# Kernel tuning notes

Measured on AMD Instinct MI355X. Metric: run time of the kernel, lower is better.

## Reference

```python
import jax, jax.numpy as jnp
import numpy as np

N = 100000   # nodes
E = 1600000  # edges per relation (avg in-degree 16)
D = 128      # gcn_hidden (in_feat == out_feat)
R = 2        # relations: forward_edge, backward_edge


def setup_inputs() -> dict:
    key = jax.random.key(0)
    ks = jax.random.split(key, 8)
    x = jax.random.normal(ks[0], (N, D), dtype=jnp.float32)
    src_fwd = jax.random.randint(ks[1], (E,), 0, N, dtype=jnp.int32)
    dst_fwd = jax.random.randint(ks[2], (E,), 0, N, dtype=jnp.int32)
    src_bwd = jax.random.randint(ks[3], (E,), 0, N, dtype=jnp.int32)
    dst_bwd = jax.random.randint(ks[4], (E,), 0, N, dtype=jnp.int32)
    # xavier_uniform with relu gain sqrt(2)
    gain = np.sqrt(2.0)
    lim_rel = gain * np.sqrt(6.0 / (D + D))
    rel_weight = jax.random.uniform(ks[5], (R, D, D), minval=-lim_rel, maxval=lim_rel, dtype=jnp.float32)
    loop_weight = jax.random.uniform(ks[6], (D, D), minval=-lim_rel, maxval=lim_rel, dtype=jnp.float32)
    h_bias = jnp.zeros((D,), dtype=jnp.float32)
    return {
        'x': x,
        'src_fwd': src_fwd, 'dst_fwd': dst_fwd,
        'src_bwd': src_bwd, 'dst_bwd': dst_bwd,
        'rel_weight': rel_weight, 'loop_weight': loop_weight, 'h_bias': h_bias,
    }


def _rel_conv(x, src, dst, W):
    # dgl GraphConv(norm='right', weight per relation): scatter-sum src feats to
    # dst, divide by clamped in-degree, then matmul W (in_feat == out_feat so
    # order of matmul vs aggregation is mathematically equivalent).
    msg = x[src]                                            # [E, D] gather
    agg = jax.ops.segment_sum(msg, dst, num_segments=N)     # [N, D] scatter-add
    deg = jax.ops.segment_sum(jnp.ones((src.shape[0],), x.dtype), dst, num_segments=N)
    agg = agg / jnp.clip(deg, 1.0)[:, None]                 # right norm, deg clamp(min=1)
    return agg @ W                                          # [N, D]


def reference(x, src_fwd, dst_fwd, src_bwd, dst_bwd, rel_weight, loop_weight, h_bias):
    h = _rel_conv(x, src_fwd, dst_fwd, rel_weight[0])
    h = h + _rel_conv(x, src_bwd, dst_bwd, rel_weight[1])   # HeteroGraphConv sums per-relation results
    h = h + x @ loop_weight                                 # self loop
    h = h + h_bias                                          # bias
    h = jax.nn.relu(h)                                      # activation
    return h                                                # dropout is identity in eval
```

## Files before the change

### kernel.cpp

```cpp
#include <hip/hip_runtime.h>
#include <hip/hip_bf16.h>


#define DFEAT 128
#define CH2 4096
#define PSH 6
#define NBMAX 3200
#define CAPB 1536
#define NPACK 24

typedef __attribute__((ext_vector_type(8))) short short8v;
typedef __attribute__((ext_vector_type(4))) float float4v;
typedef __attribute__((ext_vector_type(2))) unsigned int u2v;
typedef __attribute__((ext_vector_type(4))) unsigned short ushort4v;

__global__ __launch_bounds__(256) void front_kernel(
        const float4v* __restrict__ x4, ushort4v* __restrict__ xb4, int n4,
        const int* __restrict__ src0, const int* __restrict__ dst0,
        const int* __restrict__ src1, const int* __restrict__ dst1,
        int* __restrict__ cursor, unsigned* __restrict__ binned,
        const float* __restrict__ wrel, const float* __restrict__ wloop,
        unsigned short* __restrict__ wb,
        int N, int E, int nbin) {
    __shared__ unsigned cntp[NBMAX / 2];
    __shared__ int base[NBMAX];
    int tid = threadIdx.x;
    int bid = blockIdx.x;

    if (bid < nbin) {
        auto ldp = [&](int i) {
            int r = (i >= E) ? 1 : 0;
            int e = i - r * E;
            int t = r ? dst1[e] : dst0[e];
            return r * N + t;
        };
        auto lds_ = [&](int i) {
            int r = (i >= E) ? 1 : 0;
            int e = i - r * E;
            return r ? src1[e] : src0[e];
        };
        for (int i = tid; i < NBMAX / 2; i += 256) cntp[i] = 0;
        __syncthreads();
        int lo = bid * CH2, hi = min(2 * E, lo + CH2);
        for (int ii = lo + tid; ii < hi; ii += 1024) {
            int p0 = ldp(ii);
            int p1 = (ii + 256 < hi) ? ldp(ii + 256) : -1;
            int p2 = (ii + 512 < hi) ? ldp(ii + 512) : -1;
            int p3 = (ii + 768 < hi) ? ldp(ii + 768) : -1;
            int b0 = p0 >> PSH;
            atomicAdd(&cntp[b0 >> 1], (b0 & 1) ? 0x10000u : 1u);
            if (p1 >= 0) { int b1 = p1 >> PSH; atomicAdd(&cntp[b1 >> 1], (b1 & 1) ? 0x10000u : 1u); }
            if (p2 >= 0) { int b2 = p2 >> PSH; atomicAdd(&cntp[b2 >> 1], (b2 & 1) ? 0x10000u : 1u); }
            if (p3 >= 0) { int b3 = p3 >> PSH; atomicAdd(&cntp[b3 >> 1], (b3 & 1) ? 0x10000u : 1u); }
        }
        __syncthreads();
        for (int b = tid; b < NBMAX; b += 256) {
            int c = (int)((cntp[b >> 1] >> ((b & 1) * 16)) & 0xFFFFu);
            if (c) base[b] = b * CAPB + atomicAdd(&cursor[b], c);
        }
        __syncthreads();
        for (int ii = lo + tid; ii < hi; ii += 1024) {
            int p0 = ldp(ii);             int s0 = lds_(ii);
            int i1 = ii + 256, i2 = ii + 512, i3 = ii + 768;
            int p1 = (i1 < hi) ? ldp(i1) : -1;  int s1 = (i1 < hi) ? lds_(i1) : 0;
            int p2 = (i2 < hi) ? ldp(i2) : -1;  int s2 = (i2 < hi) ? lds_(i2) : 0;
            int p3 = (i3 < hi) ? ldp(i3) : -1;  int s3 = (i3 < hi) ? lds_(i3) : 0;
            { int slot = atomicAdd(&base[p0 >> PSH], 1);
              binned[slot] = ((unsigned)(p0 & 63) << 17) | (unsigned)s0; }
            if (p1 >= 0) { int slot = atomicAdd(&base[p1 >> PSH], 1);
                           binned[slot] = ((unsigned)(p1 & 63) << 17) | (unsigned)s1; }
            if (p2 >= 0) { int slot = atomicAdd(&base[p2 >> PSH], 1);
                           binned[slot] = ((unsigned)(p2 & 63) << 17) | (unsigned)s2; }
            if (p3 >= 0) { int slot = atomicAdd(&base[p3 >> PSH], 1);
                           binned[slot] = ((unsigned)(p3 & 63) << 17) | (unsigned)s3; }
        }
    } else if (bid < nbin + NPACK) {
        int t = (bid - nbin) * 256 + tid;
        if (t < 12 * 8 * 64) {
            int lane = t & 63;
            int kbase = (t >> 9) * 32 + (lane >> 4) * 8;
            int col = (((t >> 6) & 7) << 4) + (lane & 15);
            unsigned short tmp[8];
#pragma unroll
            for (int j = 0; j < 8; ++j) {
                int k = kbase + j;
                float v = (k < 256) ? wrel[k * DFEAT + col]
                                    : wloop[(k - 256) * DFEAT + col];
                tmp[j] = __hip_bfloat16_raw(__float2bfloat16(v)).x;
            }
            *(ushort4*)(wb + t * 8)     = make_ushort4(tmp[0], tmp[1], tmp[2], tmp[3]);
            *(ushort4*)(wb + t * 8 + 4) = make_ushort4(tmp[4], tmp[5], tmp[6], tmp[7]);
        }
    } else {
        int cb = bid - nbin - NPACK;
#pragma unroll
        for (int k = 0; k < 4; ++k) {
            int i = cb * 1024 + k * 256 + tid;
            if (i < n4) {
                float4v v = __builtin_nontemporal_load(x4 + i);
                ushort4v o;
                o[0] = __hip_bfloat16_raw(__float2bfloat16(v[0])).x;
                o[1] = __hip_bfloat16_raw(__float2bfloat16(v[1])).x;
                o[2] = __hip_bfloat16_raw(__float2bfloat16(v[2])).x;
                o[3] = __hip_bfloat16_raw(__float2bfloat16(v[3])).x;
                xb4[i] = o;
            }
        }
    }
}

#define CONSUME(Q0, Q1, Q2, Q3) {                                              \
    a[0] += __uint_as_float(Q0[0] << 16) + __uint_as_float(Q1[0] << 16)        \
          + __uint_as_float(Q2[0] << 16) + __uint_as_float(Q3[0] << 16);       \
    a[1] += __uint_as_float(Q0[0] & 0xffff0000u) + __uint_as_float(Q1[0] & 0xffff0000u) \
          + __uint_as_float(Q2[0] & 0xffff0000u) + __uint_as_float(Q3[0] & 0xffff0000u); \
    a[2] += __uint_as_float(Q0[1] << 16) + __uint_as_float(Q1[1] << 16)        \
          + __uint_as_float(Q2[1] << 16) + __uint_as_float(Q3[1] << 16);       \
    a[3] += __uint_as_float(Q0[1] & 0xffff0000u) + __uint_as_float(Q1[1] & 0xffff0000u) \
          + __uint_as_float(Q2[1] & 0xffff0000u) + __uint_as_float(Q3[1] & 0xffff0000u); }

__global__ __launch_bounds__(128) void agg_kernel(
        const u2v* __restrict__ xb2,
        const unsigned* __restrict__ binned,
        const int* __restrict__ cursor,
        unsigned short* __restrict__ aggb, int N, int M) {
    __shared__ unsigned ebuf[CAPB];
    __shared__ int cnt[64], cur[64], rs[64];
    int tid = threadIdx.x;
    int b = blockIdx.x;
    int total = min(cursor[b], CAPB);
    const unsigned* seg = binned + (size_t)b * CAPB;
    int P0 = b << PSH;
    int hw = tid >> 5, lane = tid & 31;

    if (tid < 64) cnt[tid] = 0;
    __syncthreads();
    for (int i = tid; i < total; i += 128)
        atomicAdd(&cnt[seg[i] >> 17], 1);
    __syncthreads();
    if (tid < 64) {
        int c = cnt[tid];
        int inc = c;
#pragma unroll
        for (int off = 1; off < 64; off <<= 1) {
            int t2 = __shfl_up(inc, off);
            if (tid >= off) inc += t2;
        }
        rs[tid] = inc - c;
        cur[tid] = inc - c;
    }
    __syncthreads();
    for (int i = tid; i < total; i += 128) {
        unsigned v = seg[i];
        int slot = atomicAdd(&cur[v >> 17], 1);
        ebuf[slot] = v & 0x1FFFFu;
    }
    __syncthreads();

    for (int pi = 0; pi < 16; ++pi) {
        int pl = hw * 16 + pi;
        int s0 = rs[pl], c = cnt[pl];
        float4v a = (float4v){0.f, 0.f, 0.f, 0.f};
        int e = 0;
        if (c >= 8) {
            u2v A0 = xb2[(size_t)ebuf[s0]     * 32 + lane];
            u2v B0 = xb2[(size_t)ebuf[s0 + 1] * 32 + lane];
            u2v C0 = xb2[(size_t)ebuf[s0 + 2] * 32 + lane];
            u2v D0 = xb2[(size_t)ebuf[s0 + 3] * 32 + lane];
            u2v A1 = xb2[(size_t)ebuf[s0 + 4] * 32 + lane];
            u2v B1 = xb2[(size_t)ebuf[s0 + 5] * 32 + lane];
            u2v C1 = xb2[(size_t)ebuf[s0 + 6] * 32 + lane];
            u2v D1 = xb2[(size_t)ebuf[s0 + 7] * 32 + lane];
            for (e = 8; e + 4 <= c; e += 4) {
                u2v nA = xb2[(size_t)ebuf[s0 + e]     * 32 + lane];
                u2v nB = xb2[(size_t)ebuf[s0 + e + 1] * 32 + lane];
                u2v nC = xb2[(size_t)ebuf[s0 + e + 2] * 32 + lane];
                u2v nD = xb2[(size_t)ebuf[s0 + e + 3] * 32 + lane];
                CONSUME(A0, B0, C0, D0);
                A0 = A1; B0 = B1; C0 = C1; D0 = D1;
                A1 = nA; B1 = nB; C1 = nC; D1 = nD;
            }
            CONSUME(A0, B0, C0, D0);
            CONSUME(A1, B1, C1, D1);
        } else if (c >= 4) {
            u2v A0 = xb2[(size_t)ebuf[s0]     * 32 + lane];
            u2v B0 = xb2[(size_t)ebuf[s0 + 1] * 32 + lane];
            u2v C0 = xb2[(size_t)ebuf[s0 + 2] * 32 + lane];
            u2v D0 = xb2[(size_t)ebuf[s0 + 3] * 32 + lane];
            CONSUME(A0, B0, C0, D0);
            e = 4;
        }
        for (; e < c; ++e) {
            int s = ebuf[s0 + e];
            u2v g = xb2[(size_t)s * 32 + lane];
            a[0] += __uint_as_float(g[0] << 16);
            a[1] += __uint_as_float(g[0] & 0xffff0000u);
            a[2] += __uint_as_float(g[1] << 16);
            a[3] += __uint_as_float(g[1] & 0xffff0000u);
        }
        int pg = P0 + pl;
        if (pg < M) {
            float inv = 1.0f / (float)max(c, 1);
            ushort4v w;
            w[0] = __hip_bfloat16_raw(__float2bfloat16(a[0] * inv)).x;
            w[1] = __hip_bfloat16_raw(__float2bfloat16(a[1] * inv)).x;
            w[2] = __hip_bfloat16_raw(__float2bfloat16(a[2] * inv)).x;
            w[3] = __hip_bfloat16_raw(__float2bfloat16(a[3] * inv)).x;
            __builtin_nontemporal_store(
                w, (ushort4v*)(aggb + (size_t)pg * DFEAT + 4 * lane));
        }
    }
}

__global__ __launch_bounds__(256) void mfma_gemm_kernel(
        const unsigned short* __restrict__ aggb,
        const unsigned short* __restrict__ xb,
        const unsigned short* __restrict__ wb,
        const float* __restrict__ bias,
        float* __restrict__ out, int N) {
    int tid = threadIdx.x;
    int wv = tid >> 6, lane = tid & 63;
    int R0 = blockIdx.x * 128 + wv * 32;
    int mrow = lane & 15, quad = lane >> 4;

    float4v acc[2][8];
#pragma unroll
    for (int rt = 0; rt < 2; ++rt)
#pragma unroll
        for (int ct = 0; ct < 8; ++ct) acc[rt][ct] = (float4v){0.f, 0.f, 0.f, 0.f};

    int n0 = min(R0 + mrow, N - 1);
    int n1 = min(R0 + 16 + mrow, N - 1);

#pragma unroll
    for (int kc = 0; kc < 12; ++kc) {
        int off = (kc & 3) * 32 + quad * 8;
        const unsigned short* s0;
        const unsigned short* s1;
        if (kc < 4)      { s0 = aggb + (size_t)n0 * DFEAT;       s1 = aggb + (size_t)n1 * DFEAT; }
        else if (kc < 8) { s0 = aggb + (size_t)(N + n0) * DFEAT; s1 = aggb + (size_t)(N + n1) * DFEAT; }
        else             { s0 = xb + (size_t)n0 * DFEAT;         s1 = xb + (size_t)n1 * DFEAT; }
        short8v a0 = *(const short8v*)(s0 + off);
        short8v a1 = *(const short8v*)(s1 + off);
#pragma unroll
        for (int ct = 0; ct < 8; ++ct) {
            short8v bfr = *(const short8v*)(wb + (((kc * 8 + ct) << 6) + lane) * 8);
            acc[0][ct] = __builtin_amdgcn_mfma_f32_16x16x32_bf16(a0, bfr, acc[0][ct], 0, 0, 0);
            acc[1][ct] = __builtin_amdgcn_mfma_f32_16x16x32_bf16(a1, bfr, acc[1][ct], 0, 0, 0);
        }
    }

#pragma unroll
    for (int ct = 0; ct < 8; ++ct) {
        int col = ct * 16 + mrow;
        float bv = bias[col];
#pragma unroll
        for (int rt = 0; rt < 2; ++rt) {
#pragma unroll
            for (int i = 0; i < 4; ++i) {
                int row = R0 + rt * 16 + quad * 4 + i;
                if (row < N)
                    __builtin_nontemporal_store(fmaxf(acc[rt][ct][i] + bv, 0.f),
                                                out + (size_t)row * DFEAT + col);
            }
        }
    }
}

extern "C" void kernel_launch(void* const* d_in, const int* in_sizes, int n_in,
                              void* d_out, int out_size, void* d_ws, size_t ws_size,
                              hipStream_t stream) {
    const float* x      = (const float*)d_in[0];
    const int* src_fwd  = (const int*)d_in[1];
    const int* dst_fwd  = (const int*)d_in[2];
    const int* src_bwd  = (const int*)d_in[3];
    const int* dst_bwd  = (const int*)d_in[4];
    const float* wrel   = (const float*)d_in[5];
    const float* wloop  = (const float*)d_in[6];
    const float* hbias  = (const float*)d_in[7];
    float* out          = (float*)d_out;

    int N = in_sizes[0] / DFEAT;
    int E = in_sizes[1];
    int M = 2 * N;
    int TE = 2 * E;
    int NB = (M + 63) / 64;

    unsigned short* wb   = (unsigned short*)d_ws;
    unsigned* binned     = (unsigned*)(wb + 12 * 8 * 64 * 8);
    unsigned short* xb   = (unsigned short*)(binned + (size_t)NB * CAPB);
    unsigned short* aggb = xb + (size_t)(N + 1) * DFEAT;
    int* cursor          = (int*)(aggb + (size_t)M * DFEAT);

    int n4 = N * (DFEAT / 4);
    int nconv = (n4 + 1023) / 1024;
    int nbin = (TE + CH2 - 1) / CH2;

    (void)hipMemsetAsync(cursor, 0, NB * sizeof(int), stream);

    front_kernel<<<nbin + NPACK + nconv, 256, 0, stream>>>(
        (const float4v*)x, (ushort4v*)xb, n4,
        src_fwd, dst_fwd, src_bwd, dst_bwd,
        cursor, binned, wrel, wloop, wb, N, E, nbin);

    agg_kernel<<<NB, 128, 0, stream>>>(
        (const u2v*)xb, binned, cursor, aggb, N, M);

    mfma_gemm_kernel<<<(N + 127) / 128, 256, 0, stream>>>(
        aggb, xb, wb, hbias, out, N);
}
```

Before: 345.6 us.

## Fuse neighbor aggregation with MFMA GEMM via shared-memory tile

Merges the aggregation and GEMM kernels into one kernel. Each block handles 64 nodes: for each relation it aggregates the bin into an LDS bf16 tile, then runs MFMA against that relation's weights, and finally adds the self-loop term from xb. The bf16 aggregate buffer is no longer written to or read back from global memory, and one launch is removed. In exchange each block has more serial phases and barriers, grid size falls to about 1563 blocks of 256 threads, and the per-row relation padding changes to Npad so bins align with node tiles.

```diff
diff --git a/kernel.cpp b/kernel.cpp
--- a/kernel.cpp
+++ b/kernel.cpp
@@ -21,7 +21,7 @@
         int* __restrict__ cursor, unsigned* __restrict__ binned,
         const float* __restrict__ wrel, const float* __restrict__ wloop,
         unsigned short* __restrict__ wb,
-        int N, int E, int nbin) {
+        int Np, int E, int nbin) {
     __shared__ unsigned cntp[NBMAX / 2];
     __shared__ int base[NBMAX];
     int tid = threadIdx.x;
@@ -32,7 +32,7 @@
             int r = (i >= E) ? 1 : 0;
             int e = i - r * E;
             int t = r ? dst1[e] : dst0[e];
-            return r * N + t;
+            return r * Np + t;
         };
         auto lds_ = [&](int i) {
             int r = (i >= E) ? 1 : 0;
@@ -119,134 +119,128 @@
     a[3] += __uint_as_float(Q0[1] & 0xffff0000u) + __uint_as_float(Q1[1] & 0xffff0000u) \
           + __uint_as_float(Q2[1] & 0xffff0000u) + __uint_as_float(Q3[1] & 0xffff0000u); }
 
-__global__ __launch_bounds__(128) void agg_kernel(
+__global__ __launch_bounds__(256) void aggmm_kernel(
         const u2v* __restrict__ xb2,
+        const unsigned short* __restrict__ xb,
         const unsigned* __restrict__ binned,
         const int* __restrict__ cursor,
-        unsigned short* __restrict__ aggb, int N, int M) {
+        const unsigned short* __restrict__ wb,
+        const float* __restrict__ bias,
+        float* __restrict__ out, int N, int NBH) {
     __shared__ unsigned ebuf[CAPB];
+    __shared__ __align__(16) unsigned short Atile[64][136];
     __shared__ int cnt[64], cur[64], rs[64];
     int tid = threadIdx.x;
-    int b = blockIdx.x;
-    int total = min(cursor[b], CAPB);
-    const unsigned* seg = binned + (size_t)b * CAPB;
-    int P0 = b << PSH;
+    int g = blockIdx.x;
     int hw = tid >> 5, lane = tid & 31;
-
-    if (tid < 64) cnt[tid] = 0;
-    __syncthreads();
-    for (int i = tid; i < total; i += 128)
-        atomicAdd(&cnt[seg[i] >> 17], 1);
-    __syncthreads();
-    if (tid < 64) {
-        int c = cnt[tid];
-        int inc = c;
-#pragma unroll
-        for (int off = 1; off < 64; off <<= 1) {
-            int t2 = __shfl_up(inc, off);
-            if (tid >= off) inc += t2;
-        }
-        rs[tid] = inc - c;
-        cur[tid] = inc - c;
-    }
-    __syncthreads();
-    for (int i = tid; i < total; i += 128) {
-        unsigned v = seg[i];
-        int slot = atomicAdd(&cur[v >> 17], 1);
-        ebuf[slot] = v & 0x1FFFFu;
-    }
-    __syncthreads();
-
-    for (int pi = 0; pi < 16; ++pi) {
-        int pl = hw * 16 + pi;
-        int s0 = rs[pl], c = cnt[pl];
-        float4v a = (float4v){0.f, 0.f, 0.f, 0.f};
-        int e = 0;
-        if (c >= 8) {
-            u2v A0 = xb2[(size_t)ebuf[s0]     * 32 + lane];
-            u2v B0 = xb2[(size_t)ebuf[s0 + 1] * 32 + lane];
-            u2v C0 = xb2[(size_t)ebuf[s0 + 2] * 32 + lane];
-            u2v D0 = xb2[(size_t)ebuf[s0 + 3] * 32 + lane];
-            u2v A1 = xb2[(size_t)ebuf[s0 + 4] * 32 + lane];
-            u2v B1 = xb2[(size_t)ebuf[s0 + 5] * 32 + lane];
-            u2v C1 = xb2[(size_t)ebuf[s0 + 6] * 32 + lane];
-            u2v D1 = xb2[(size_t)ebuf[s0 + 7] * 32 + lane];
-            for (e = 8; e + 4 <= c; e += 4) {
-                u2v nA = xb2[(size_t)ebuf[s0 + e]     * 32 + lane];
-                u2v nB = xb2[(size_t)ebuf[s0 + e + 1] * 32 + lane];
-                u2v nC = xb2[(size_t)ebuf[s0 + e + 2] * 32 + lane];
-                u2v nD = xb2[(size_t)ebuf[s0 + e + 3] * 32 + lane];
+    int wv = tid >> 6, l64 = tid & 63;
+    int mrow = l64 & 15, quad = l64 >> 4;
+
+    float4v acc[8];
+#pragma unroll
+    for (int ct = 0; ct < 8; ++ct) acc[ct] = (float4v){0.f, 0.f, 0.f, 0.f};
+
+    for (int rel = 0; rel < 2; ++rel) {
+        int b = rel ? (NBH + g) : g;
+        int total = min(cursor[b], CAPB);
+        const unsigned* seg = binned + (size_t)b * CAPB;
+
+        if (tid < 64) cnt[tid] = 0;
+        __syncthreads();
+        for (int i = tid; i < total; i += 256)
+            atomicAdd(&cnt[seg[i] >> 17], 1);
+        __syncthreads();
+        if (tid < 64) {
+            int c = cnt[tid];
+            int inc = c;
+#pragma unroll
+            for (int off = 1; off < 64; off <<= 1) {
+                int t2 = __shfl_up(inc, off);
+                if (tid >= off) inc += t2;
+            }
+            rs[tid] = inc - c;
+            cur[tid] = inc - c;
+        }
+        __syncthreads();
+        for (int i = tid; i < total; i += 256) {
+            unsigned v = seg[i];
+            int slot = atomicAdd(&cur[v >> 17], 1);
+            ebuf[slot] = v & 0x1FFFFu;
+        }
+        __syncthreads();
+
+        for (int pi = 0; pi < 8; ++pi) {
+            int pl = hw * 8 + pi;
+            int s0 = rs[pl], c = cnt[pl];
+            float4v a = (float4v){0.f, 0.f, 0.f, 0.f};
+            int e = 0;
+            if (c >= 8) {
+                u2v A0 = xb2[(size_t)ebuf[s0]     * 32 + lane];
+                u2v B0 = xb2[(size_t)ebuf[s0 + 1] * 32 + lane];
+                u2v C0 = xb2[(size_t)ebuf[s0 + 2] * 32 + lane];
+                u2v D0 = xb2[(size_t)ebuf[s0 + 3] * 32 + lane];
+                u2v A1 = xb2[(size_t)ebuf[s0 + 4] * 32 + lane];
+                u2v B1 = xb2[(size_t)ebuf[s0 + 5] * 32 + lane];
+                u2v C1 = xb2[(size_t)ebuf[s0 + 6] * 32 + lane];
+                u2v D1 = xb2[(size_t)ebuf[s0 + 7] * 32 + lane];
+                for (e = 8; e + 4 <= c; e += 4) {
+                    u2v nA = xb2[(size_t)ebuf[s0 + e]     * 32 + lane];
+                    u2v nB = xb2[(size_t)ebuf[s0 + e + 1] * 32 + lane];
+                    u2v nC = xb2[(size_t)ebuf[s0 + e + 2] * 32 + lane];
+                    u2v nD = xb2[(size_t)ebuf[s0 + e + 3] * 32 + lane];
+                    CONSUME(A0, B0, C0, D0);
+                    A0 = A1; B0 = B1; C0 = C1; D0 = D1;
+                    A1 = nA; B1 = nB; C1 = nC; D1 = nD;
+                }
                 CONSUME(A0, B0, C0, D0);
-                A0 = A1; B0 = B1; C0 = C1; D0 = D1;
-                A1 = nA; B1 = nB; C1 = nC; D1 = nD;
-            }
-            CONSUME(A0, B0, C0, D0);
-            CONSUME(A1, B1, C1, D1);
-        } else if (c >= 4) {
-            u2v A0 = xb2[(size_t)ebuf[s0]     * 32 + lane];
-            u2v B0 = xb2[(size_t)ebuf[s0 + 1] * 32 + lane];
-            u2v C0 = xb2[(size_t)ebuf[s0 + 2] * 32 + lane];
-            u2v D0 = xb2[(size_t)ebuf[s0 + 3] * 32 + lane];
-            CONSUME(A0, B0, C0, D0);
-            e = 4;
-        }
-        for (; e < c; ++e) {
-            int s = ebuf[s0 + e];
-            u2v g = xb2[(size_t)s * 32 + lane];
-            a[0] += __uint_as_float(g[0] << 16);
-            a[1] += __uint_as_float(g[0] & 0xffff0000u);
-            a[2] += __uint_as_float(g[1] << 16);
-            a[3] += __uint_as_float(g[1] & 0xffff0000u);
-        }
-        int pg = P0 + pl;
-        if (pg < M) {
+                CONSUME(A1, B1, C1, D1);
+            } else if (c >= 4) {
+                u2v A0 = xb2[(size_t)ebuf[s0]     * 32 + lane];
+                u2v B0 = xb2[(size_t)ebuf[s0 + 1] * 32 + lane];
+                u2v C0 = xb2[(size_t)ebuf[s0 + 2] * 32 + lane];
+                u2v D0 = xb2[(size_t)ebuf[s0 + 3] * 32 + lane];
+                CONSUME(A0, B0, C0, D0);
+                e = 4;
+            }
+            for (; e < c; ++e) {
+                int s = ebuf[s0 + e];
+                u2v gq = xb2[(size_t)s * 32 + lane];
+                a[0] += __uint_as_float(gq[0] << 16);
+                a[1] += __uint_as_float(gq[0] & 0xffff0000u);
+                a[2] += __uint_as_float(gq[1] << 16);
+                a[3] += __uint_as_float(gq[1] & 0xffff0000u);
+            }
             float inv = 1.0f / (float)max(c, 1);
             ushort4v w;
             w[0] = __hip_bfloat16_raw(__float2bfloat16(a[0] * inv)).x;
             w[1] = __hip_bfloat16_raw(__float2bfloat16(a[1] * inv)).x;
             w[2] = __hip_bfloat16_raw(__float2bfloat16(a[2] * inv)).x;
             w[3] = __hip_bfloat16_raw(__float2bfloat16(a[3] * inv)).x;
-            __builtin_nontemporal_store(
-                w, (ushort4v*)(aggb + (size_t)pg * DFEAT + 4 * lane));
-        }
-    }
-}
-
-__global__ __launch_bounds__(256) void mfma_gemm_kernel(
-        const unsigned short* __restrict__ aggb,
-        const unsigned short* __restrict__ xb,
-        const unsigned short* __restrict__ wb,
-        const float* __restrict__ bias,
-        float* __restrict__ out, int N) {
-    int tid = threadIdx.x;
-    int wv = tid >> 6, lane = tid & 63;
-    int R0 = blockIdx.x * 128 + wv * 32;
-    int mrow = lane & 15, quad = lane >> 4;
-
-    float4v acc[2][8];
-#pragma unroll
-    for (int rt = 0; rt < 2; ++rt)
-#pragma unroll
-        for (int ct = 0; ct < 8; ++ct) acc[rt][ct] = (float4v){0.f, 0.f, 0.f, 0.f};
-
-    int n0 = min(R0 + mrow, N - 1);
-    int n1 = min(R0 + 16 + mrow, N - 1);
-
-#pragma unroll
-    for (int kc = 0; kc < 12; ++kc) {
-        int off = (kc & 3) * 32 + quad * 8;
-        const unsigned short* s0;
-        const unsigned short* s1;
-        if (kc < 4)      { s0 = aggb + (size_t)n0 * DFEAT;       s1 = aggb + (size_t)n1 * DFEAT; }
-        else if (kc < 8) { s0 = aggb + (size_t)(N + n0) * DFEAT; s1 = aggb + (size_t)(N + n1) * DFEAT; }
-        else             { s0 = xb + (size_t)n0 * DFEAT;         s1 = xb + (size_t)n1 * DFEAT; }
-        short8v a0 = *(const short8v*)(s0 + off);
-        short8v a1 = *(const short8v*)(s1 + off);
+            *(ushort4v*)&Atile[pl][4 * lane] = w;
+        }
+        __syncthreads();
+
+#pragma unroll
+        for (int kc4 = 0; kc4 < 4; ++kc4) {
+            int kc = rel * 4 + kc4;
+            short8v a0 = *(const short8v*)&Atile[wv * 16 + mrow][kc4 * 32 + quad * 8];
+#pragma unroll
+            for (int ct = 0; ct < 8; ++ct) {
+                short8v bfr = *(const short8v*)(wb + (((kc * 8 + ct) << 6) + l64) * 8);
+                acc[ct] = __builtin_amdgcn_mfma_f32_16x16x32_bf16(a0, bfr, acc[ct], 0, 0, 0);
+            }
+        }
+        __syncthreads();
+    }
+
+    int n0 = min(g * 64 + wv * 16 + mrow, N - 1);
+#pragma unroll
+    for (int kc = 8; kc < 12; ++kc) {
+        short8v a0 = *(const short8v*)(xb + (size_t)n0 * DFEAT + (kc & 3) * 32 + quad * 8);
 #pragma unroll
         for (int ct = 0; ct < 8; ++ct) {
-            short8v bfr = *(const short8v*)(wb + (((kc * 8 + ct) << 6) + lane) * 8);
-            acc[0][ct] = __builtin_amdgcn_mfma_f32_16x16x32_bf16(a0, bfr, acc[0][ct], 0, 0, 0);
-            acc[1][ct] = __builtin_amdgcn_mfma_f32_16x16x32_bf16(a1, bfr, acc[1][ct], 0, 0, 0);
+            short8v bfr = *(const short8v*)(wb + (((kc * 8 + ct) << 6) + l64) * 8);
+            acc[ct] = __builtin_amdgcn_mfma_f32_16x16x32_bf16(a0, bfr, acc[ct], 0, 0, 0);
         }
     }
 
@@ -255,14 +249,11 @@
         int col = ct * 16 + mrow;
         float bv = bias[col];
 #pragma unroll
-        for (int rt = 0; rt < 2; ++rt) {
-#pragma unroll
-            for (int i = 0; i < 4; ++i) {
-                int row = R0 + rt * 16 + quad * 4 + i;
-                if (row < N)
-                    __builtin_nontemporal_store(fmaxf(acc[rt][ct][i] + bv, 0.f),
-                                                out + (size_t)row * DFEAT + col);
-            }
+        for (int i = 0; i < 4; ++i) {
+            int row = g * 64 + wv * 16 + quad * 4 + i;
+            if (row < N)
+                __builtin_nontemporal_store(fmaxf(acc[ct][i] + bv, 0.f),
+                                            out + (size_t)row * DFEAT + col);
         }
     }
 }
@@ -282,15 +273,15 @@
 
     int N = in_sizes[0] / DFEAT;
     int E = in_sizes[1];
-    int M = 2 * N;
     int TE = 2 * E;
-    int NB = (M + 63) / 64;
+    int Npad = (N + 63) & ~63;
+    int NBH = Npad >> 6;
+    int NB = 2 * NBH;
 
     unsigned short* wb   = (unsigned short*)d_ws;
     unsigned* binned     = (unsigned*)(wb + 12 * 8 * 64 * 8);
     unsigned short* xb   = (unsigned short*)(binned + (size_t)NB * CAPB);
-    unsigned short* aggb = xb + (size_t)(N + 1) * DFEAT;
-    int* cursor          = (int*)(aggb + (size_t)M * DFEAT);
+    int* cursor          = (int*)(xb + (size_t)(N + 1) * DFEAT);
 
     int n4 = N * (DFEAT / 4);
     int nconv = (n4 + 1023) / 1024;
@@ -301,11 +292,8 @@
     front_kernel<<<nbin + NPACK + nconv, 256, 0, stream>>>(
         (const float4v*)x, (ushort4v*)xb, n4,
         src_fwd, dst_fwd, src_bwd, dst_bwd,
-        cursor, binned, wrel, wloop, wb, N, E, nbin);
-
-    agg_kernel<<<NB, 128, 0, stream>>>(
-        (const u2v*)xb, binned, cursor, aggb, N, M);
-
-    mfma_gemm_kernel<<<(N + 127) / 128, 256, 0, stream>>>(
-        aggb, xb, wb, hbias, out, N);
+        cursor, binned, wrel, wloop, wb, Npad, E, nbin);
+
+    aggmm_kernel<<<NBH, 256, 0, stream>>>(
+        (const u2v*)xb, xb, binned, cursor, wb, hbias, out, N, NBH);
 }
```

Result: slower. 357.7 us (+3.5%).

## Split aggregation launch in two and halve GEMM rows per block

Applied to the files above, without the earlier changes.

The aggregation kernel is now launched as two back-to-back grids over the two halves of the bins, using a new block offset parameter. The GEMM kernel drops from two 16-row tiles per wave to one, so each block covers 64 rows and the grid doubles. The aim is to raise GEMM occupancy and parallelism by cutting accumulator registers, and to change how aggregation blocks are scheduled. In exchange the weight fragments are reloaded twice as often per output row, and the split adds an extra kernel launch with a serialization point between the two halves.

```diff
diff --git a/kernel.cpp b/kernel.cpp
--- a/kernel.cpp
+++ b/kernel.cpp
@@ -123,11 +123,11 @@
         const u2v* __restrict__ xb2,
         const unsigned* __restrict__ binned,
         const int* __restrict__ cursor,
-        unsigned short* __restrict__ aggb, int N, int M) {
+        unsigned short* __restrict__ aggb, int N, int M, int bstart) {
     __shared__ unsigned ebuf[CAPB];
     __shared__ int cnt[64], cur[64], rs[64];
     int tid = threadIdx.x;
-    int b = blockIdx.x;
+    int b = bstart + blockIdx.x;
     int total = min(cursor[b], CAPB);
     const unsigned* seg = binned + (size_t)b * CAPB;
     int P0 = b << PSH;
@@ -220,33 +220,27 @@
         float* __restrict__ out, int N) {
     int tid = threadIdx.x;
     int wv = tid >> 6, lane = tid & 63;
-    int R0 = blockIdx.x * 128 + wv * 32;
+    int R0 = blockIdx.x * 64 + wv * 16;
     int mrow = lane & 15, quad = lane >> 4;
 
-    float4v acc[2][8];
-#pragma unroll
-    for (int rt = 0; rt < 2; ++rt)
-#pragma unroll
-        for (int ct = 0; ct < 8; ++ct) acc[rt][ct] = (float4v){0.f, 0.f, 0.f, 0.f};
+    float4v acc[8];
+#pragma unroll
+    for (int ct = 0; ct < 8; ++ct) acc[ct] = (float4v){0.f, 0.f, 0.f, 0.f};
 
     int n0 = min(R0 + mrow, N - 1);
-    int n1 = min(R0 + 16 + mrow, N - 1);
 
 #pragma unroll
     for (int kc = 0; kc < 12; ++kc) {
         int off = (kc & 3) * 32 + quad * 8;
         const unsigned short* s0;
-        const unsigned short* s1;
-        if (kc < 4)      { s0 = aggb + (size_t)n0 * DFEAT;       s1 = aggb + (size_t)n1 * DFEAT; }
-        else if (kc < 8) { s0 = aggb + (size_t)(N + n0) * DFEAT; s1 = aggb + (size_t)(N + n1) * DFEAT; }
-        else             { s0 = xb + (size_t)n0 * DFEAT;         s1 = xb + (size_t)n1 * DFEAT; }
+        if (kc < 4)      s0 = aggb + (size_t)n0 * DFEAT;
+        else if (kc < 8) s0 = aggb + (size_t)(N + n0) * DFEAT;
+        else             s0 = xb + (size_t)n0 * DFEAT;
         short8v a0 = *(const short8v*)(s0 + off);
-        short8v a1 = *(const short8v*)(s1 + off);
 #pragma unroll
         for (int ct = 0; ct < 8; ++ct) {
             short8v bfr = *(const short8v*)(wb + (((kc * 8 + ct) << 6) + lane) * 8);
-            acc[0][ct] = __builtin_amdgcn_mfma_f32_16x16x32_bf16(a0, bfr, acc[0][ct], 0, 0, 0);
-            acc[1][ct] = __builtin_amdgcn_mfma_f32_16x16x32_bf16(a1, bfr, acc[1][ct], 0, 0, 0);
+            acc[ct] = __builtin_amdgcn_mfma_f32_16x16x32_bf16(a0, bfr, acc[ct], 0, 0, 0);
         }
     }
 
@@ -255,14 +249,11 @@
         int col = ct * 16 + mrow;
         float bv = bias[col];
 #pragma unroll
-        for (int rt = 0; rt < 2; ++rt) {
-#pragma unroll
-            for (int i = 0; i < 4; ++i) {
-                int row = R0 + rt * 16 + quad * 4 + i;
-                if (row < N)
-                    __builtin_nontemporal_store(fmaxf(acc[rt][ct][i] + bv, 0.f),
-                                                out + (size_t)row * DFEAT + col);
-            }
+        for (int i = 0; i < 4; ++i) {
+            int row = R0 + quad * 4 + i;
+            if (row < N)
+                __builtin_nontemporal_store(fmaxf(acc[ct][i] + bv, 0.f),
+                                            out + (size_t)row * DFEAT + col);
         }
     }
 }
@@ -303,9 +294,13 @@
         src_fwd, dst_fwd, src_bwd, dst_bwd,
         cursor, binned, wrel, wloop, wb, N, E, nbin);
 
-    agg_kernel<<<NB, 128, 0, stream>>>(
-        (const u2v*)xb, binned, cursor, aggb, N, M);
-
-    mfma_gemm_kernel<<<(N + 127) / 128, 256, 0, stream>>>(
+    int c0 = (NB + 1) / 2;
+    int c1 = NB - c0;
+    agg_kernel<<<c0, 128, 0, stream>>>(
+        (const u2v*)xb, binned, cursor, aggb, N, M, 0);
+    agg_kernel<<<c1, 128, 0, stream>>>(
+        (const u2v*)xb, binned, cursor, aggb, N, M, c0);
+
+    mfma_gemm_kernel<<<(N + 63) / 64, 256, 0, stream>>>(
         aggb, xb, wb, hbias, out, N);
 }
```

Measured after the change: 368.5 us. 6.6% more time.
